# Performance work log

Hardware: AMD Instinct MI355X
Metric: run time of the kernel (lower is better)

The kernel has to match this reference:

```python
import jax, jax.numpy as jnp
import numpy as np

EPS = 1e-5  # torch InstanceNorm1d default

def _inorm(x):
    # instance norm over length dim per (batch, channel), no affine, biased var
    m = jnp.mean(x, axis=-1, keepdims=True)
    v = jnp.var(x, axis=-1, keepdims=True)
    return (x - m) * jax.lax.rsqrt(v + EPS)

def _conv1x1(W, b, x):
    # kernel-size-1 Conv1d == per-position linear: [O,C] x [B,C,T] -> [B,O,T]
    return jnp.einsum('oc,bct->bot', W, x) + b[None, :, None]

def setup_inputs() -> dict:
    key = jax.random.key(0)
    ks = jax.random.split(key, 10)
    B, C, T = 4, 512, 2048
    s = 1.0 / np.sqrt(C)  # conv1d default init scale
    return {
        'x_c': jax.random.normal(ks[0], (B, C, T), jnp.float32),
        'x_s': jax.random.normal(ks[1], (B, C, T), jnp.float32),
        'Wn': jax.random.normal(ks[2], (C, C), jnp.float32) * s,
        'bn': jax.random.normal(ks[3], (C,), jnp.float32) * s,
        'Wm': jax.random.normal(ks[4], (C, C), jnp.float32) * s,
        'bm': jax.random.normal(ks[5], (C,), jnp.float32) * s,
        'Wl': jax.random.normal(ks[6], (C, C), jnp.float32) * s,
        'bl': jax.random.normal(ks[7], (C,), jnp.float32) * s,
        'Wo': jax.random.normal(ks[8], (C, C), jnp.float32) * s,
        'bo': jax.random.normal(ks[9], (C,), jnp.float32) * s,
    }

def reference(x_c, x_s, Wn, bn, Wm, bm, Wl, bl, Wo, bo):
    Mn = _conv1x1(Wn, bn, _inorm(x_c))           # [B,C,Tc]
    Mm = _conv1x1(Wm, bm, _inorm(x_s))           # [B,C,Ts]
    A = jax.nn.softmax(jnp.einsum('bct,bcs->bts', Mn, Mm), axis=-1)  # [B,Tc,Ts]
    Ml = _conv1x1(Wl, bl, x_s)                   # [B,C,Ts]
    Mo = jnp.einsum('bcs,bts->bct', Ml, A)       # [B,C,Tc]
    return _conv1x1(Wo, bo, Mo) + x_c
```

## Files before the change

kernel.cpp:

```cpp
#include <hip/hip_runtime.h>
#include <hip/hip_bf16.h>
#include <stdint.h>

typedef _Float16 f16;
typedef _Float16 f16x8 __attribute__((ext_vector_type(8)));
typedef _Float16 f16x4 __attribute__((ext_vector_type(4)));
typedef float    f32x4 __attribute__((ext_vector_type(4)));

#define BB 4
#define CC 512
#define TT 2048

__device__ __forceinline__ void gload16(const void* g, void* l) {
  __builtin_amdgcn_global_load_lds((const __attribute__((address_space(1))) void*)g,
                                   (__attribute__((address_space(3))) void*)l, 16, 0, 0);
}

__device__ __forceinline__ void xcd_swizzle(int& bx, int& by, int& bz) {
  int gx = gridDim.x, gy = gridDim.y;
  int F = bx + gx * (by + gy * bz);
  int q = (gx * gy * gridDim.z) >> 3;
  int l = (F & 7) * q + (F >> 3);
  bx = l % gx; by = (l / gx) % gy; bz = l / (gx * gy);
}

__global__ __launch_bounds__(256) void transpose_kernel(
    const float* __restrict__ xc, const float* __restrict__ xs,
    f16* __restrict__ xcT, f16* __restrict__ xsT,
    float* __restrict__ sumc, float* __restrict__ sqc,
    float* __restrict__ sums_, float* __restrict__ sqs) {
  const int b = blockIdx.z & 3, which = blockIdx.z >> 2;
  const float* src = (which ? xs : xc) + (long)b * CC * TT;
  f16* dst = (which ? xsT : xcT) + (long)b * TT * CC;
  float* sumP = (which ? sums_ : sumc) + b * CC;
  float* sqP  = (which ? sqs   : sqc ) + b * CC;
  const int t0 = blockIdx.x * 64, c0 = blockIdx.y * 64;
  __shared__ float tile[64][65];
  const int tid = threadIdx.x;
  #pragma unroll
  for (int it = 0; it < 4; ++it) {
    int s = it * 256 + tid, r = s >> 4, q = s & 15;
    float4 v = *(const float4*)&src[(long)(c0 + r) * TT + t0 + q * 4];
    tile[r][q*4+0] = v.x; tile[r][q*4+1] = v.y; tile[r][q*4+2] = v.z; tile[r][q*4+3] = v.w;
    float ps = v.x + v.y + v.z + v.w;
    float pq = v.x*v.x + v.y*v.y + v.z*v.z + v.w*v.w;
    #pragma unroll
    for (int o = 8; o; o >>= 1) { ps += __shfl_xor(ps, o); pq += __shfl_xor(pq, o); }
    if ((tid & 15) == 0) {
      atomicAdd(&sumP[c0 + r], ps);
      atomicAdd(&sqP [c0 + r], pq);
    }
  }
  __syncthreads();
  #pragma unroll
  for (int it = 0; it < 4; ++it) {
    int s = it * 256 + tid, r = s >> 4, q = s & 15;
    f16x4 o;
    o[0] = (f16)tile[q*4+0][r]; o[1] = (f16)tile[q*4+1][r];
    o[2] = (f16)tile[q*4+2][r]; o[3] = (f16)tile[q*4+3][r];
    *(f16x4*)&dst[(long)(t0 + r) * CC + c0 + q * 4] = o;
  }
}

__global__ __launch_bounds__(256) void prepw_kernel(
    const float* __restrict__ W, const float* __restrict__ bias,
    const float* __restrict__ sum, const float* __restrict__ sq,
    f16* __restrict__ Weff, float* __restrict__ beff) {
  const int o = blockIdx.x, b = blockIdx.y, tid = threadIdx.x;
  float acc = 0.f;
  #pragma unroll
  for (int j = 0; j < 2; ++j) {
    int c = tid + j * 256;
    float mean = sum[b * CC + c] * (1.f / TT);
    float var  = sq [b * CC + c] * (1.f / TT) - mean * mean;
    float iv = 1.0f / sqrtf(var + 1e-5f);
    float wv = W[(long)o * CC + c] * iv;
    Weff[((long)b * CC + o) * CC + c] = (f16)wv;
    acc += wv * mean;
  }
  #pragma unroll
  for (int off = 32; off; off >>= 1) acc += __shfl_xor(acc, off);
  __shared__ float red[4];
  if ((tid & 63) == 0) red[tid >> 6] = acc;
  __syncthreads();
  if (tid == 0) beff[b * CC + o] = bias[o] - (red[0] + red[1] + red[2] + red[3]);
}

__global__ __launch_bounds__(256) void f2h_kernel(const float* __restrict__ src,
                                                  f16* __restrict__ dst) {
  long i = ((long)blockIdx.x * 256 + threadIdx.x) * 8;
  float4 a = *(const float4*)&src[i], d = *(const float4*)&src[i + 4];
  f16x8 o;
  o[0]=(f16)a.x; o[1]=(f16)a.y; o[2]=(f16)a.z; o[3]=(f16)a.w;
  o[4]=(f16)d.x; o[5]=(f16)d.y; o[6]=(f16)d.z; o[7]=(f16)d.w;
  *(f16x8*)&dst[i] = o;
}

__global__ __launch_bounds__(256) void softmax_kernel(f16* __restrict__ S) {
  f16* p = S + ((long)blockIdx.y * TT + blockIdx.x) * TT;
  const int tid = threadIdx.x;
  f16x8 v8 = ((const f16x8*)p)[tid];
  float v[8];
  #pragma unroll
  for (int j = 0; j < 8; ++j) v[j] = (float)v8[j];
  float m = v[0];
  #pragma unroll
  for (int j = 1; j < 8; ++j) m = fmaxf(m, v[j]);
  #pragma unroll
  for (int o = 32; o; o >>= 1) m = fmaxf(m, __shfl_xor(m, o));
  __shared__ float red[4], red2[4];
  if (!(tid & 63)) red[tid >> 6] = m;
  __syncthreads();
  m = fmaxf(fmaxf(red[0], red[1]), fmaxf(red[2], red[3]));
  float e[8], sum = 0.f;
  #pragma unroll
  for (int j = 0; j < 8; ++j) { e[j] = __expf(v[j] - m); sum += e[j]; }
  #pragma unroll
  for (int o = 32; o; o >>= 1) sum += __shfl_xor(sum, o);
  if (!(tid & 63)) red2[tid >> 6] = sum;
  __syncthreads();
  sum = red2[0] + red2[1] + red2[2] + red2[3];
  float is = 1.f / sum;
  f16x8 o8;
  #pragma unroll
  for (int j = 0; j < 8; ++j) o8[j] = (f16)(e[j] * is);
  ((f16x8*)p)[tid] = o8;
}

template <int BM, int NT, typename OutT>
__device__ __forceinline__ void gemm_core(
    const f16* __restrict__ A, int lda,
    const f16* __restrict__ BT, int ldb,
    OutT* __restrict__ C, int ldc,
    const float* __restrict__ bias,
    const float* __restrict__ resid, int ldres,
    int bm, int bn, int K, bool transw) {

  constexpr int CA = BM * 8 / NT;
  constexpr int CB = 128 * 8 / NT;
  constexpr int ABUFB = BM * 128;
  constexpr int BBUFB = 128 * 128;

  __shared__ f16 sA[2 * BM * 64];
  __shared__ f16 sB[2 * 128 * 64];

  const int tid = threadIdx.x, lane = tid & 63, wv = tid >> 6;
  const int wr = wv >> 1, wc = wv & 1;

  const char* gAp[CA]; int lAo[CA];
  #pragma unroll
  for (int i = 0; i < CA; ++i) {
    int cid = tid + i * NT, row = cid >> 3;
    int colb = ((cid & 7) * 16) ^ ((row & 7) << 4);
    gAp[i] = (const char*)A + (long)(bm + row) * lda * 2 + colb;
    lAo[i] = cid * 16;
  }
  const char* gBp[CB]; int lBo[CB];
  #pragma unroll
  for (int i = 0; i < CB; ++i) {
    int cid = tid + i * NT, row = cid >> 3;
    int colb = ((cid & 7) * 16) ^ ((row & 7) << 4);
    gBp[i] = (const char*)BT + (long)(bn + row) * ldb * 2 + colb;
    lBo[i] = cid * 16;
  }

  const int lm = lane & 15, lkb = (lane >> 4) * 16, sw = (lane & 7) << 4;
  int aoff[2][2], boff[4][2];
  #pragma unroll
  for (int mi = 0; mi < 2; ++mi) {
    int r = wr * 32 + mi * 16 + lm;
    #pragma unroll
    for (int kk = 0; kk < 2; ++kk)
      aoff[mi][kk] = r * 128 + ((kk * 64 + lkb) ^ sw);
  }
  #pragma unroll
  for (int ni = 0; ni < 4; ++ni) {
    int r = wc * 64 + ni * 16 + lm;
    #pragma unroll
    for (int kk = 0; kk < 2; ++kk)
      boff[ni][kk] = r * 128 + ((kk * 64 + lkb) ^ sw);
  }

  f32x4 acc[2][4] = {};
  const int nk = K >> 6;

  #pragma unroll
  for (int i = 0; i < CA; ++i) gload16(gAp[i], (char*)sA + lAo[i]);
  #pragma unroll
  for (int i = 0; i < CB; ++i) gload16(gBp[i], (char*)sB + lBo[i]);
  __syncthreads();

  int cur = 0;
  for (int kt = 0; kt < nk; ++kt) {
    if (kt + 1 < nk) {
      long kb = (long)(kt + 1) * 128;
      int na = (cur ^ 1) * ABUFB, nb = (cur ^ 1) * BBUFB;
      #pragma unroll
      for (int i = 0; i < CA; ++i) gload16(gAp[i] + kb, (char*)sA + na + lAo[i]);
      #pragma unroll
      for (int i = 0; i < CB; ++i) gload16(gBp[i] + kb, (char*)sB + nb + lBo[i]);
    }
    const char* pa = (const char*)sA + cur * ABUFB;
    const char* pb = (const char*)sB + cur * BBUFB;
    f16x8 af[2][2], bf[4][2];
    #pragma unroll
    for (int mi = 0; mi < 2; ++mi)
      #pragma unroll
      for (int kk = 0; kk < 2; ++kk)
        af[mi][kk] = *(const f16x8*)(pa + aoff[mi][kk]);
    #pragma unroll
    for (int ni = 0; ni < 4; ++ni)
      #pragma unroll
      for (int kk = 0; kk < 2; ++kk)
        bf[ni][kk] = *(const f16x8*)(pb + boff[ni][kk]);
    #pragma unroll
    for (int kk = 0; kk < 2; ++kk)
      #pragma unroll
      for (int mi = 0; mi < 2; ++mi)
        #pragma unroll
        for (int ni = 0; ni < 4; ++ni)
          acc[mi][ni] = __builtin_amdgcn_mfma_f32_16x16x32_f16(af[mi][kk], bf[ni][kk], acc[mi][ni], 0, 0, 0);
    __syncthreads();
    cur ^= 1;
  }

  struct alignas(4 * sizeof(OutT)) Pack4 { OutT v[4]; };
  const int rr = (lane >> 4) * 4;
  #pragma unroll
  for (int mi = 0; mi < 2; ++mi) {
    int m0 = bm + wr * 32 + mi * 16 + rr;
    #pragma unroll
    for (int ni = 0; ni < 4; ++ni) {
      int n0 = bn + wc * 64 + ni * 16 + lm;
      f32x4 v = acc[mi][ni];
      float vals[4];
      #pragma unroll
      for (int r = 0; r < 4; ++r) {
        vals[r] = v[r];
        if (bias)  vals[r] += bias[m0 + r];
        if (resid) vals[r] += resid[(long)(m0 + r) * ldres + n0];
      }
      if (transw) {
        Pack4 pk;
        #pragma unroll
        for (int r = 0; r < 4; ++r) pk.v[r] = (OutT)vals[r];
        *(Pack4*)&C[(long)n0 * ldc + m0] = pk;
      } else {
        #pragma unroll
        for (int r = 0; r < 4; ++r)
          C[(long)(m0 + r) * ldc + n0] = (OutT)vals[r];
      }
    }
  }
}

__global__ __launch_bounds__(512) void conv_kernel(
    const f16* __restrict__ xcT, const f16* __restrict__ xsT,
    const f16* __restrict__ WnE, const float* __restrict__ bnE,
    const f16* __restrict__ WmE, const float* __restrict__ bmE,
    const f16* __restrict__ WlB, const float* __restrict__ bl,
    f16* __restrict__ MnT, f16* __restrict__ MmT, f16* __restrict__ Ml) {
  int bx = blockIdx.x, by = blockIdx.y, bz = blockIdx.z;
  xcd_swizzle(bx, by, bz);
  const int cid = bz >> 2, b = bz & 3;
  const f16* A; const float* bias; const f16* B; f16* C; int ldc; bool transw;
  if (cid == 0)      { A = WnE + (long)b*CC*CC; bias = bnE + b*CC; B = xcT + (long)b*TT*CC; C = MnT + (long)b*TT*CC; ldc = CC; transw = true; }
  else if (cid == 1) { A = WmE + (long)b*CC*CC; bias = bmE + b*CC; B = xsT + (long)b*TT*CC; C = MmT + (long)b*TT*CC; ldc = CC; transw = true; }
  else               { A = WlB;                 bias = bl;         B = xsT + (long)b*TT*CC; C = Ml  + (long)b*CC*TT; ldc = TT; transw = false; }
  gemm_core<128, 512, f16>(A, CC, B, CC, C, ldc, bias, nullptr, 0,
                           by * 128, bx * 128, CC, transw);
}

__global__ __launch_bounds__(512) void sgemm_kernel(
    const f16* __restrict__ MnT, const f16* __restrict__ MmT, f16* __restrict__ S) {
  int bx = blockIdx.x, by = blockIdx.y, bz = blockIdx.z;
  xcd_swizzle(bx, by, bz);
  gemm_core<128, 512, f16>(MnT + (long)bz*TT*CC, CC, MmT + (long)bz*TT*CC, CC,
                           S + (long)bz*TT*TT, TT, nullptr, nullptr, 0,
                           by * 128, bx * 128, CC, false);
}

__global__ __launch_bounds__(256) void pv_kernel(
    const f16* __restrict__ P, const f16* __restrict__ Ml, f16* __restrict__ MoT) {
  int bx = blockIdx.x, by = blockIdx.y, bz = blockIdx.z;
  xcd_swizzle(bx, by, bz);
  gemm_core<64, 256, f16>(P + (long)bz*TT*TT, TT, Ml + (long)bz*CC*TT, TT,
                          MoT + (long)bz*TT*CC, CC, nullptr, nullptr, 0,
                          by * 64, bx * 128, TT, false);
}

__global__ __launch_bounds__(256) void out_kernel(
    const f16* __restrict__ WoB, const f16* __restrict__ MoT,
    const float* __restrict__ bo, const float* __restrict__ xc, float* __restrict__ out) {
  int bx = blockIdx.x, by = blockIdx.y, bz = blockIdx.z;
  xcd_swizzle(bx, by, bz);
  gemm_core<64, 256, float>(WoB, CC, MoT + (long)bz*TT*CC, CC,
                            out + (long)bz*CC*TT, TT, bo, xc + (long)bz*CC*TT, TT,
                            by * 64, bx * 128, CC, false);
}

extern "C" void kernel_launch(void* const* d_in, const int* in_sizes, int n_in,
                              void* d_out, int out_size, void* d_ws, size_t ws_size,
                              hipStream_t stream) {
  const float* x_c = (const float*)d_in[0];
  const float* x_s = (const float*)d_in[1];
  const float* Wn  = (const float*)d_in[2];
  const float* bn  = (const float*)d_in[3];
  const float* Wm  = (const float*)d_in[4];
  const float* bm  = (const float*)d_in[5];
  const float* Wl  = (const float*)d_in[6];
  const float* bl  = (const float*)d_in[7];
  const float* Wo  = (const float*)d_in[8];
  const float* bo  = (const float*)d_in[9];
  float* out = (float*)d_out;

  char* w = (char*)d_ws;
  auto alloc = [&](size_t bytes) { char* p = w; w += (bytes + 255) & ~(size_t)255; return p; };
  float* sumc = (float*)alloc(BB * CC * 4);
  float* sqc  = (float*)alloc(BB * CC * 4);
  float* sums_ = (float*)alloc(BB * CC * 4);
  float* sqs  = (float*)alloc(BB * CC * 4);
  float* bnE  = (float*)alloc(BB * CC * 4);
  float* bmE  = (float*)alloc(BB * CC * 4);
  f16* WnE = (f16*)alloc((size_t)BB * CC * CC * 2);
  f16* WmE = (f16*)alloc((size_t)BB * CC * CC * 2);
  f16* WlB = (f16*)alloc((size_t)CC * CC * 2);
  f16* WoB = (f16*)alloc((size_t)CC * CC * 2);
  f16* xcT = (f16*)alloc((size_t)BB * TT * CC * 2);
  f16* xsT = (f16*)alloc((size_t)BB * TT * CC * 2);
  f16* MnT = (f16*)alloc((size_t)BB * TT * CC * 2);
  f16* MmT = (f16*)alloc((size_t)BB * TT * CC * 2);
  f16* Ml  = (f16*)alloc((size_t)BB * CC * TT * 2);
  f16* S   = (f16*)alloc((size_t)BB * TT * TT * 2);
  f16* MoT = (f16*)alloc((size_t)BB * TT * CC * 2);

  hipMemsetAsync(sumc, 0, (size_t)4 * BB * CC * 4, stream);

  transpose_kernel<<<dim3(TT / 64, CC / 64, BB * 2), dim3(256), 0, stream>>>(
      x_c, x_s, xcT, xsT, sumc, sqc, sums_, sqs);
  prepw_kernel<<<dim3(CC, BB), dim3(256), 0, stream>>>(Wn, bn, sumc, sqc, WnE, bnE);
  prepw_kernel<<<dim3(CC, BB), dim3(256), 0, stream>>>(Wm, bm, sums_, sqs, WmE, bmE);
  f2h_kernel<<<dim3(CC * CC / (256 * 8)), dim3(256), 0, stream>>>(Wl, WlB);
  f2h_kernel<<<dim3(CC * CC / (256 * 8)), dim3(256), 0, stream>>>(Wo, WoB);

  conv_kernel<<<dim3(16, 4, 12), dim3(512), 0, stream>>>(
      xcT, xsT, WnE, bnE, WmE, bmE, WlB, bl, MnT, MmT, Ml);
  sgemm_kernel<<<dim3(16, 16, BB), dim3(512), 0, stream>>>(MnT, MmT, S);
  softmax_kernel<<<dim3(TT, BB), dim3(256), 0, stream>>>(S);
  pv_kernel<<<dim3(4, 32, BB), dim3(256), 0, stream>>>(S, Ml, MoT);
  out_kernel<<<dim3(16, 8, BB), dim3(256), 0, stream>>>(WoB, MoT, bo, x_c, out);
}
```

Baseline: 234.8 us.

## Use explicit vmcnt waits in GEMM loop, merge prep launches, enlarge PV tiles

```diff
diff --git a/kernel.cpp b/kernel.cpp
--- a/kernel.cpp
+++ b/kernel.cpp
@@ -14,6 +14,13 @@
 __device__ __forceinline__ void gload16(const void* g, void* l) {
   __builtin_amdgcn_global_load_lds((const __attribute__((address_space(1))) void*)g,
                                    (__attribute__((address_space(3))) void*)l, 16, 0, 0);
+}
+
+template <int N>
+__device__ __forceinline__ void s_wait_vmcnt() {
+  if constexpr (N == 0)      asm volatile("s_waitcnt vmcnt(0)" ::: "memory");
+  else if constexpr (N == 4) asm volatile("s_waitcnt vmcnt(4)" ::: "memory");
+  else if constexpr (N == 6) asm volatile("s_waitcnt vmcnt(6)" ::: "memory");
 }
 
 __device__ __forceinline__ void xcd_swizzle(int& bx, int& by, int& bz) {
@@ -63,10 +70,19 @@
 }
 
 __global__ __launch_bounds__(256) void prepw_kernel(
-    const float* __restrict__ W, const float* __restrict__ bias,
-    const float* __restrict__ sum, const float* __restrict__ sq,
-    f16* __restrict__ Weff, float* __restrict__ beff) {
-  const int o = blockIdx.x, b = blockIdx.y, tid = threadIdx.x;
+    const float* __restrict__ Wn, const float* __restrict__ bn,
+    const float* __restrict__ Wm, const float* __restrict__ bm_,
+    const float* __restrict__ sumc, const float* __restrict__ sqc,
+    const float* __restrict__ sums_, const float* __restrict__ sqs,
+    f16* __restrict__ WnE, float* __restrict__ bnE,
+    f16* __restrict__ WmE, float* __restrict__ bmE) {
+  const int o = blockIdx.x, b = blockIdx.y, which = blockIdx.z, tid = threadIdx.x;
+  const float* W    = which ? Wm : Wn;
+  const float* bias = which ? bm_ : bn;
+  const float* sum  = which ? sums_ : sumc;
+  const float* sq   = which ? sqs : sqc;
+  f16* Weff   = which ? WmE : WnE;
+  float* beff = which ? bmE : bnE;
   float acc = 0.f;
   #pragma unroll
   for (int j = 0; j < 2; ++j) {
@@ -86,8 +102,12 @@
   if (tid == 0) beff[b * CC + o] = bias[o] - (red[0] + red[1] + red[2] + red[3]);
 }
 
-__global__ __launch_bounds__(256) void f2h_kernel(const float* __restrict__ src,
-                                                  f16* __restrict__ dst) {
+__global__ __launch_bounds__(256) void f2h_kernel(const float* __restrict__ s0,
+                                                  f16* __restrict__ d0,
+                                                  const float* __restrict__ s1,
+                                                  f16* __restrict__ d1) {
+  const float* src = blockIdx.y ? s1 : s0;
+  f16* dst = blockIdx.y ? d1 : d0;
   long i = ((long)blockIdx.x * 256 + threadIdx.x) * 8;
   float4 a = *(const float4*)&src[i], d = *(const float4*)&src[i + 4];
   f16x8 o;
@@ -138,6 +158,7 @@
 
   constexpr int CA = BM * 8 / NT;
   constexpr int CB = 128 * 8 / NT;
+  constexpr int LOADS = CA + CB;
   constexpr int ABUFB = BM * 128;
   constexpr int BBUFB = 128 * 128;
 
@@ -188,20 +209,23 @@
   for (int i = 0; i < CA; ++i) gload16(gAp[i], (char*)sA + lAo[i]);
   #pragma unroll
   for (int i = 0; i < CB; ++i) gload16(gBp[i], (char*)sB + lBo[i]);
-  __syncthreads();
-
-  int cur = 0;
+
   for (int kt = 0; kt < nk; ++kt) {
     if (kt + 1 < nk) {
       long kb = (long)(kt + 1) * 128;
-      int na = (cur ^ 1) * ABUFB, nb = (cur ^ 1) * BBUFB;
+      int na = ((kt + 1) & 1) * ABUFB, nb = ((kt + 1) & 1) * BBUFB;
       #pragma unroll
       for (int i = 0; i < CA; ++i) gload16(gAp[i] + kb, (char*)sA + na + lAo[i]);
       #pragma unroll
       for (int i = 0; i < CB; ++i) gload16(gBp[i] + kb, (char*)sB + nb + lBo[i]);
+      s_wait_vmcnt<LOADS>();
+    } else {
+      s_wait_vmcnt<0>();
     }
-    const char* pa = (const char*)sA + cur * ABUFB;
-    const char* pb = (const char*)sB + cur * BBUFB;
+    __builtin_amdgcn_s_barrier();
+
+    const char* pa = (const char*)sA + (kt & 1) * ABUFB;
+    const char* pb = (const char*)sB + (kt & 1) * BBUFB;
     f16x8 af[2][2], bf[4][2];
     #pragma unroll
     for (int mi = 0; mi < 2; ++mi)
@@ -220,8 +244,8 @@
         #pragma unroll
         for (int ni = 0; ni < 4; ++ni)
           acc[mi][ni] = __builtin_amdgcn_mfma_f32_16x16x32_f16(af[mi][kk], bf[ni][kk], acc[mi][ni], 0, 0, 0);
-    __syncthreads();
-    cur ^= 1;
+
+    __builtin_amdgcn_s_barrier();
   }
 
   struct alignas(4 * sizeof(OutT)) Pack4 { OutT v[4]; };
@@ -280,13 +304,13 @@
                            by * 128, bx * 128, CC, false);
 }
 
-__global__ __launch_bounds__(256) void pv_kernel(
+__global__ __launch_bounds__(512) void pv_kernel(
     const f16* __restrict__ P, const f16* __restrict__ Ml, f16* __restrict__ MoT) {
   int bx = blockIdx.x, by = blockIdx.y, bz = blockIdx.z;
   xcd_swizzle(bx, by, bz);
-  gemm_core<64, 256, f16>(P + (long)bz*TT*TT, TT, Ml + (long)bz*CC*TT, TT,
-                          MoT + (long)bz*TT*CC, CC, nullptr, nullptr, 0,
-                          by * 64, bx * 128, TT, false);
+  gemm_core<128, 512, f16>(P + (long)bz*TT*TT, TT, Ml + (long)bz*CC*TT, TT,
+                           MoT + (long)bz*TT*CC, CC, nullptr, nullptr, 0,
+                           by * 128, bx * 128, TT, false);
 }
 
 __global__ __launch_bounds__(256) void out_kernel(
@@ -316,12 +340,12 @@
 
   char* w = (char*)d_ws;
   auto alloc = [&](size_t bytes) { char* p = w; w += (bytes + 255) & ~(size_t)255; return p; };
-  float* sumc = (float*)alloc(BB * CC * 4);
-  float* sqc  = (float*)alloc(BB * CC * 4);
+  float* sumc  = (float*)alloc(BB * CC * 4);
+  float* sqc   = (float*)alloc(BB * CC * 4);
   float* sums_ = (float*)alloc(BB * CC * 4);
-  float* sqs  = (float*)alloc(BB * CC * 4);
-  float* bnE  = (float*)alloc(BB * CC * 4);
-  float* bmE  = (float*)alloc(BB * CC * 4);
+  float* sqs   = (float*)alloc(BB * CC * 4);
+  float* bnE   = (float*)alloc(BB * CC * 4);
+  float* bmE   = (float*)alloc(BB * CC * 4);
   f16* WnE = (f16*)alloc((size_t)BB * CC * CC * 2);
   f16* WmE = (f16*)alloc((size_t)BB * CC * CC * 2);
   f16* WlB = (f16*)alloc((size_t)CC * CC * 2);
@@ -338,15 +362,14 @@
 
   transpose_kernel<<<dim3(TT / 64, CC / 64, BB * 2), dim3(256), 0, stream>>>(
       x_c, x_s, xcT, xsT, sumc, sqc, sums_, sqs);
-  prepw_kernel<<<dim3(CC, BB), dim3(256), 0, stream>>>(Wn, bn, sumc, sqc, WnE, bnE);
-  prepw_kernel<<<dim3(CC, BB), dim3(256), 0, stream>>>(Wm, bm, sums_, sqs, WmE, bmE);
-  f2h_kernel<<<dim3(CC * CC / (256 * 8)), dim3(256), 0, stream>>>(Wl, WlB);
-  f2h_kernel<<<dim3(CC * CC / (256 * 8)), dim3(256), 0, stream>>>(Wo, WoB);
+  prepw_kernel<<<dim3(CC, BB, 2), dim3(256), 0, stream>>>(
+      Wn, bn, Wm, bm, sumc, sqc, sums_, sqs, WnE, bnE, WmE, bmE);
+  f2h_kernel<<<dim3(CC * CC / (256 * 8), 2), dim3(256), 0, stream>>>(Wl, WlB, Wo, WoB);
 
   conv_kernel<<<dim3(16, 4, 12), dim3(512), 0, stream>>>(
       xcT, xsT, WnE, bnE, WmE, bmE, WlB, bl, MnT, MmT, Ml);
   sgemm_kernel<<<dim3(16, 16, BB), dim3(512), 0, stream>>>(MnT, MmT, S);
   softmax_kernel<<<dim3(TT, BB), dim3(256), 0, stream>>>(S);
-  pv_kernel<<<dim3(4, 32, BB), dim3(256), 0, stream>>>(S, Ml, MoT);
+  pv_kernel<<<dim3(4, 16, BB), dim3(512), 0, stream>>>(S, Ml, MoT);
   out_kernel<<<dim3(16, 8, BB), dim3(256), 0, stream>>>(WoB, MoT, bo, x_c, out);
 }
```

Result: faster. 219.2 us (-6.6%).
